# Optimization experiments

Hardware: AMD Instinct MI355X
Metric: run time of the kernel (lower is better)

Reference implementation:

```python
import jax, jax.numpy as jnp
import numpy as np
import math

D_MODEL = 1024
N_HEADS = 16
HEAD_DIM = D_MODEL // N_HEADS
B = 2
S = 2048

def setup_inputs() -> dict:
    key = jax.random.key(0)
    ks = jax.random.split(key, 5)
    x = jax.random.normal(ks[0], (B, S, D_MODEL), dtype=jnp.float32)
    # causal lower-triangular mask, broadcastable to [B, H, S, S]
    mask = jnp.tril(jnp.ones((S, S), dtype=bool))[None, None, :, :]
    # qkv_proj: Linear(d_model, 3*d_model); out_proj: Linear(d_model, d_model)
    lim_qkv = 1.0 / math.sqrt(D_MODEL)
    Wqkv = jax.random.uniform(ks[1], (D_MODEL, 3 * D_MODEL), minval=-lim_qkv, maxval=lim_qkv, dtype=jnp.float32)
    bqkv = jax.random.uniform(ks[2], (3 * D_MODEL,), minval=-lim_qkv, maxval=lim_qkv, dtype=jnp.float32)
    Wo = jax.random.uniform(ks[3], (D_MODEL, D_MODEL), minval=-lim_qkv, maxval=lim_qkv, dtype=jnp.float32)
    bo = jax.random.uniform(ks[4], (D_MODEL,), minval=-lim_qkv, maxval=lim_qkv, dtype=jnp.float32)
    return {"x": x, "mask": mask, "Wqkv": Wqkv, "bqkv": bqkv, "Wo": Wo, "bo": bo}

def reference(x, mask, Wqkv, bqkv, Wo, bo):
    b, s, d = x.shape
    scale = math.sqrt(HEAD_DIM)
    qkv = x @ Wqkv + bqkv                                   # [b, s, 3d]
    qkv = qkv.reshape(b, s, 3, N_HEADS, HEAD_DIM)
    qkv = jnp.transpose(qkv, (2, 0, 3, 1, 4))               # [3, b, h, s, hd]
    q, k, v = qkv[0], qkv[1], qkv[2]
    scores = jnp.einsum("bhqd,bhkd->bhqk", q, k) / scale    # [b, h, s, s]
    scores = jnp.where(mask, scores, -jnp.inf)
    attn = jax.nn.softmax(scores, axis=-1)                  # dropout inactive (eval)
    out = jnp.einsum("bhqk,bhkd->bhqd", attn, v)            # [b, h, s, hd]
    out = jnp.transpose(out, (0, 2, 1, 3)).reshape(b, s, d)
    return out @ Wo + bo
```

## Files before the change

kernel.cpp:

```cpp
#include <hip/hip_runtime.h>
#include <stdint.h>

typedef __bf16 bf16x8 __attribute__((ext_vector_type(8)));
typedef float  f32x4  __attribute__((ext_vector_type(4)));

__device__ __forceinline__ float bf2f(ushort u) {
    union { uint i; float f; } v; v.i = ((uint)u) << 16; return v.f;
}
__device__ __forceinline__ ushort f2bf(float f) {
    union { uint i; float f; } v; v.f = f;
    uint i = v.i;
    uint r = (i + 0x7fffu + ((i >> 16) & 1u)) >> 16;
    return (ushort)r;
}
__device__ __forceinline__ ushort f2bf_t(float f) {
    union { uint i; float f; } v; v.f = f;
    return (ushort)(v.i >> 16);
}

#if __has_builtin(__builtin_amdgcn_exp2f)
#define EXP2F __builtin_amdgcn_exp2f
#else
#define EXP2F exp2f
#endif

__device__ __forceinline__ void gld16(const ushort* g, ushort* l) {
    __builtin_amdgcn_global_load_lds((const __attribute__((address_space(1))) uint*)g,
                                     (__attribute__((address_space(3))) uint*)l, 16, 0, 0);
}

#define D_MODEL 1024
#define N_HEADS 16
#define HEAD_DIM 64
#define BATCH 2
#define SEQ 2048
#define M_ROWS (BATCH * SEQ)
#define N_ITEMS 1024
#define SCALE_LOG2E 0.18033688f

__global__ __launch_bounds__(256) void cast_f32_bf16(
    const float* __restrict__ in, ushort* __restrict__ out, int n4)
{
    int i = blockIdx.x * 256 + threadIdx.x;
    if (i < n4) {
        float4 v = ((const float4*)in)[i];
        ushort4 o;
        o.x = f2bf(v.x); o.y = f2bf(v.y); o.z = f2bf(v.z); o.w = f2bf(v.w);
        ((ushort4*)out)[i] = o;
    }
}

__global__ __launch_bounds__(256) void transpose_f32_bf16(
    const float* __restrict__ in, ushort* __restrict__ out, int K, int N)
{
    __shared__ float tile[64][65];
    const int k0 = blockIdx.y << 6, n0 = blockIdx.x << 6;
    const int tid = threadIdx.x;
    {
        const int r  = tid >> 4;
        const int c4 = (tid & 15) * 4;
#pragma unroll
        for (int rr = 0; rr < 4; ++rr) {
            int kk = r + rr * 16;
            float4 v = *(const float4*)(in + (size_t)(k0 + kk) * N + n0 + c4);
            tile[kk][c4 + 0] = v.x; tile[kk][c4 + 1] = v.y;
            tile[kk][c4 + 2] = v.z; tile[kk][c4 + 3] = v.w;
        }
    }
    __syncthreads();
    {
        const int nn = tid & 63;
        const int ch = tid >> 6;
#pragma unroll
        for (int cc = 0; cc < 2; ++cc) {
            int k8 = (ch + cc * 4) * 8;
            ushort tmp[8] __attribute__((aligned(16)));
#pragma unroll
            for (int j = 0; j < 8; ++j) tmp[j] = f2bf(tile[k8 + j][nn]);
            *(uint4*)(out + (size_t)(n0 + nn) * K + k0 + k8) = *(const uint4*)tmp;
        }
    }
}

__global__ __launch_bounds__(256) void gemm_bt128(
    const ushort* __restrict__ A, const ushort* __restrict__ Bt,
    const float* __restrict__ bias, float* __restrict__ out,
    ushort* __restrict__ Qb, ushort* __restrict__ Kb, ushort* __restrict__ Vb,
    int M, int N, int K, int mode)
{
    __shared__ ushort smem[64 * 136];
    ushort* As = smem;
    ushort* Bs = smem + 128 * 32;
    const int tid = threadIdx.x, lane = tid & 63, w = tid >> 6;
    const int wr = w >> 1, wc = w & 1;
    const int m0 = blockIdx.y * 128, n0 = blockIdx.x * 128;
    const int quad = lane >> 4, r15 = lane & 15, q8 = quad * 8;

    f32x4 acc[4][4] = {};

    const int cb0 = w * 64;
    const int cb1 = 256 + w * 64;
    const int c0 = cb0 + lane, c1 = cb1 + lane;
    const int row0 = c0 >> 2, sc0 = (c0 & 3) * 8;
    const int row1 = c1 >> 2, sc1 = (c1 & 3) * 8;

    for (int k0 = 0; k0 < K; k0 += 32) {
        gld16(A  + (size_t)(m0 + row0) * K + k0 + sc0, As + cb0 * 8);
        gld16(A  + (size_t)(m0 + row1) * K + k0 + sc1, As + cb1 * 8);
        gld16(Bt + (size_t)(n0 + row0) * K + k0 + sc0, Bs + cb0 * 8);
        gld16(Bt + (size_t)(n0 + row1) * K + k0 + sc1, Bs + cb1 * 8);
        __syncthreads();
        bf16x8 af[4], bfv[4];
#pragma unroll
        for (int mt = 0; mt < 4; ++mt)
            af[mt] = *(const bf16x8*)&As[(wr * 64 + mt * 16 + r15) * 32 + q8];
#pragma unroll
        for (int nt = 0; nt < 4; ++nt)
            bfv[nt] = *(const bf16x8*)&Bs[(wc * 64 + nt * 16 + r15) * 32 + q8];
#pragma unroll
        for (int mt = 0; mt < 4; ++mt)
#pragma unroll
            for (int nt = 0; nt < 4; ++nt)
                acc[mt][nt] = __builtin_amdgcn_mfma_f32_16x16x32_bf16(af[mt], bfv[nt], acc[mt][nt], 0, 0, 0);
        __syncthreads();
    }

    const int q4 = quad * 4;
    float bv[4];
#pragma unroll
    for (int nt = 0; nt < 4; ++nt) bv[nt] = bias[n0 + wc * 64 + nt * 16 + r15];

    if (mode == 0) {
        ushort* Cs = smem;
#pragma unroll
        for (int h = 0; h < 2; ++h) {
            __syncthreads();
            if (wr == h) {
#pragma unroll
                for (int mt = 0; mt < 4; ++mt)
#pragma unroll
                    for (int nt = 0; nt < 4; ++nt)
#pragma unroll
                        for (int r = 0; r < 4; ++r)
                            Cs[(mt * 16 + q4 + r) * 136 + wc * 64 + nt * 16 + r15] =
                                f2bf(acc[mt][nt][r] + bv[nt]);
            }
            __syncthreads();
#pragma unroll
            for (int it = 0; it < 4; ++it) {
                int idx = it * 256 + tid;
                int row = idx >> 4, chunk = idx & 15;
                int m = m0 + h * 64 + row;
                int n = n0 + chunk * 8;
                int which = n >> 10, nh = n & 1023;
                int hh = nh >> 6, d = nh & 63;
                int b = m >> 11, s = m & 2047;
                size_t dst = (((size_t)(b * N_HEADS + hh)) * SEQ + s) * HEAD_DIM + d;
                ushort* p = (which == 0) ? Qb : ((which == 1) ? Kb : Vb);
                *(uint4*)(p + dst) = *(const uint4*)&Cs[row * 136 + chunk * 8];
            }
        }
    } else {
        float* Cf = (float*)smem;
#pragma unroll
        for (int h = 0; h < 4; ++h) {
            __syncthreads();
            if (wr == (h >> 1)) {
                const int mtb = (h & 1) * 2;
#pragma unroll
                for (int mt2 = 0; mt2 < 2; ++mt2)
#pragma unroll
                    for (int nt = 0; nt < 4; ++nt)
#pragma unroll
                        for (int r = 0; r < 4; ++r)
                            Cf[(mt2 * 16 + q4 + r) * 136 + wc * 64 + nt * 16 + r15] =
                                acc[mtb + mt2][nt][r] + bv[nt];
            }
            __syncthreads();
#pragma unroll
            for (int it = 0; it < 4; ++it) {
                int idx = it * 256 + tid;
                int row = idx >> 5, chunk = idx & 31;
                float4 v = *(const float4*)&Cf[row * 136 + chunk * 4];
                int m = m0 + h * 32 + row;
                *(float4*)(out + (size_t)m * N + n0 + chunk * 4) = v;
            }
        }
    }
}

__global__ __launch_bounds__(256) void attn_mfma(
    const ushort* __restrict__ Q, const ushort* __restrict__ K,
    const ushort* __restrict__ V, ushort* __restrict__ Out,
    int* __restrict__ counter)
{
    __shared__ ushort Ks[2][64 * 72];
    __shared__ ushort Vt[2][64 * 72];
    __shared__ ushort Ps[4][16 * 72];
    __shared__ int s_item;

    const int tid  = threadIdx.x;
    const int lane = tid & 63;
    const int w    = tid >> 6;
    const int quad = lane >> 4;
    const int r15  = lane & 15;
    const int q8   = quad * 8;

    const int srow = tid >> 2;
    const int scol = (tid & 3) * 16;
    const int kp = tid & 31;
    const int dg = tid >> 5;

    for (;;) {
        __syncthreads();
        if (tid == 0) s_item = atomicAdd(counter, 1);
        __syncthreads();
        const int item = s_item;
        if (item >= N_ITEMS) break;

        const int qblk = 31 - (item >> 5);
        const int bh   = item & 31;
        const int q0   = qblk * 64;
        const size_t base = (size_t)bh * SEQ * HEAD_DIM;
        const int wq0  = q0 + w * 16;
        const int ntiles = qblk + 1;

        bf16x8 qf[2];
        {
            const ushort* qrow = Q + base + (size_t)(wq0 + r15) * HEAD_DIM;
            qf[0] = *(const bf16x8*)(qrow + q8);
            qf[1] = *(const bf16x8*)(qrow + 32 + q8);
        }

        f32x4 o_acc[4] = {};
        float l_lane[4] = {0.f, 0.f, 0.f, 0.f};

        uint4 kr0, kr1, vr0, vr1;
        {
            const ushort* kpt = K + base + (size_t)srow * HEAD_DIM + scol;
            kr0 = *(const uint4*)kpt; kr1 = *(const uint4*)(kpt + 8);
            const ushort* vpt = V + base + (size_t)(2 * kp) * HEAD_DIM + dg * 8;
            vr0 = *(const uint4*)vpt; vr1 = *(const uint4*)(vpt + HEAD_DIM);
        }
        {
            ushort* ks = &Ks[0][0];
            *(uint4*)&ks[srow * 72 + scol]     = kr0;
            *(uint4*)&ks[srow * 72 + scol + 8] = kr1;
            const ushort* a = (const ushort*)&vr0;
            const ushort* b = (const ushort*)&vr1;
            uint* vt32 = (uint*)&Vt[0][0];
#pragma unroll
            for (int j = 0; j < 8; ++j)
                vt32[(dg * 8 + j) * 36 + ((kp + 4 * dg) & 31)] = (uint)a[j] | ((uint)b[j] << 16);
        }
        if (ntiles > 1) {
            const ushort* kpt = K + base + (size_t)(64 + srow) * HEAD_DIM + scol;
            kr0 = *(const uint4*)kpt; kr1 = *(const uint4*)(kpt + 8);
            const ushort* vpt = V + base + (size_t)(64 + 2 * kp) * HEAD_DIM + dg * 8;
            vr0 = *(const uint4*)vpt; vr1 = *(const uint4*)(vpt + HEAD_DIM);
        }

        for (int t = 0; t < ntiles; ++t) {
            __syncthreads();
            if (t + 1 < ntiles) {
                const int b1 = (t + 1) & 1;
                ushort* ks = &Ks[b1][0];
                *(uint4*)&ks[srow * 72 + scol]     = kr0;
                *(uint4*)&ks[srow * 72 + scol + 8] = kr1;
                const ushort* a = (const ushort*)&vr0;
                const ushort* b = (const ushort*)&vr1;
                uint* vt32 = (uint*)&Vt[b1][0];
#pragma unroll
                for (int j = 0; j < 8; ++j)
                    vt32[(dg * 8 + j) * 36 + ((kp + 4 * dg) & 31)] = (uint)a[j] | ((uint)b[j] << 16);
            }
            if (t + 2 < ntiles) {
                const int key2 = (t + 2) << 6;
                const ushort* kpt = K + base + (size_t)(key2 + srow) * HEAD_DIM + scol;
                kr0 = *(const uint4*)kpt; kr1 = *(const uint4*)(kpt + 8);
                const ushort* vpt = V + base + (size_t)(key2 + 2 * kp) * HEAD_DIM + dg * 8;
                vr0 = *(const uint4*)vpt; vr1 = *(const uint4*)(vpt + HEAD_DIM);
            }

            const ushort* KsB = &Ks[t & 1][0];
            const ushort* VtB = &Vt[t & 1][0];
            const bool diag = (t == ntiles - 1);
            const int ntmax = diag ? (w + 1) : 4;

            f32x4 s_acc[4];
            __builtin_amdgcn_s_setprio(1);
#pragma unroll
            for (int nt = 0; nt < 4; ++nt) {
                if (nt >= ntmax) continue;
                f32x4 z = {};
#pragma unroll
                for (int ks = 0; ks < 2; ++ks) {
                    bf16x8 kf = *(const bf16x8*)&KsB[(nt * 16 + r15) * 72 + ks * 32 + q8];
                    z = __builtin_amdgcn_mfma_f32_16x16x32_bf16(qf[ks], kf, z, 0, 0, 0);
                }
                s_acc[nt] = z;
            }
            __builtin_amdgcn_s_setprio(0);
#pragma unroll
            for (int nt = 0; nt < 4; ++nt) {
                if (nt >= ntmax) continue;
#pragma unroll
                for (int j = 0; j < 4; ++j) {
                    float e = EXP2F(s_acc[nt][j] * SCALE_LOG2E);
                    if (diag && nt == w && r15 > quad * 4 + j) e = 0.f;
                    s_acc[nt][j] = e;
                    l_lane[j] += e;
                }
            }
            ushort* pb = &Ps[w][0];
#pragma unroll
            for (int nt = 0; nt < 4; ++nt)
#pragma unroll
                for (int j = 0; j < 4; ++j)
                    pb[(quad * 4 + j) * 72 + nt * 16 + r15] =
                        (nt < ntmax) ? f2bf_t(s_acc[nt][j]) : (ushort)0;
            bf16x8 pf0 = *(const bf16x8*)&pb[r15 * 72 + q8];
            bf16x8 pf1 = *(const bf16x8*)&pb[r15 * 72 + 32 + q8];

            __builtin_amdgcn_s_setprio(1);
#pragma unroll
            for (int nt = 0; nt < 4; ++nt) {
                const int d0 = nt * 16 + r15;
                const int dsw = 4 * ((d0 >> 3) & 7);
                const int c0 = (4 * quad + dsw) & 31;
                const int c1 = (16 + 4 * quad + dsw) & 31;
                bf16x8 vf0 = *(const bf16x8*)&VtB[d0 * 72 + (c0 << 1)];
                bf16x8 vf1 = *(const bf16x8*)&VtB[d0 * 72 + (c1 << 1)];
                o_acc[nt] = __builtin_amdgcn_mfma_f32_16x16x32_bf16(pf0, vf0, o_acc[nt], 0, 0, 0);
                o_acc[nt] = __builtin_amdgcn_mfma_f32_16x16x32_bf16(pf1, vf1, o_acc[nt], 0, 0, 0);
            }
            __builtin_amdgcn_s_setprio(0);
        }

        float l_f[4];
#pragma unroll
        for (int j = 0; j < 4; ++j) {
            float l = l_lane[j];
            l += __shfl_xor(l, 1);
            l += __shfl_xor(l, 2);
            l += __shfl_xor(l, 4);
            l += __shfl_xor(l, 8);
            l_f[j] = 1.f / l;
        }
        const int b = bh >> 4, h = bh & 15;
#pragma unroll
        for (int nt = 0; nt < 4; ++nt) {
#pragma unroll
            for (int j = 0; j < 4; ++j) {
                int qg = wq0 + quad * 4 + j;
                float v = o_acc[nt][j] * l_f[j];
                Out[((size_t)(b * SEQ + qg)) * D_MODEL + h * 64 + nt * 16 + r15] = f2bf(v);
            }
        }
    }
}

extern "C" void kernel_launch(void* const* d_in, const int* in_sizes, int n_in,
                              void* d_out, int out_size, void* d_ws, size_t ws_size,
                              hipStream_t stream)
{
    const float* x    = (const float*)d_in[0];
    const float* Wqkv = (const float*)d_in[2];
    const float* bqkv = (const float*)d_in[3];
    const float* Wo   = (const float*)d_in[4];
    const float* bo   = (const float*)d_in[5];
    float* out = (float*)d_out;

    char* ws = (char*)d_ws;
    size_t off = 0;
    ushort* xb    = (ushort*)(ws + off); off += (size_t)M_ROWS * D_MODEL * 2;
    ushort* WqkvT = (ushort*)(ws + off); off += (size_t)3 * D_MODEL * D_MODEL * 2;
    ushort* WoT   = (ushort*)(ws + off); off += (size_t)D_MODEL * D_MODEL * 2;
    const size_t qkv_elems = (size_t)BATCH * N_HEADS * SEQ * HEAD_DIM;
    ushort* Qb = (ushort*)(ws + off); off += qkv_elems * 2;
    ushort* Kb = (ushort*)(ws + off); off += qkv_elems * 2;
    ushort* Vb = (ushort*)(ws + off); off += qkv_elems * 2;
    ushort* attn_out = (ushort*)(ws + off); off += (size_t)M_ROWS * D_MODEL * 2;
    int* counter = (int*)(ws + off); off += 256;

    hipMemsetAsync(counter, 0, 4, stream);

    {
        int n4 = M_ROWS * D_MODEL / 4;
        cast_f32_bf16<<<(n4 + 255) / 256, 256, 0, stream>>>(x, xb, n4);
    }

    transpose_f32_bf16<<<dim3(3 * D_MODEL / 64, D_MODEL / 64), 256, 0, stream>>>(Wqkv, WqkvT, D_MODEL, 3 * D_MODEL);
    transpose_f32_bf16<<<dim3(D_MODEL / 64, D_MODEL / 64), 256, 0, stream>>>(Wo, WoT, D_MODEL, D_MODEL);

    gemm_bt128<<<dim3(3 * D_MODEL / 128, M_ROWS / 128), 256, 0, stream>>>(
        xb, WqkvT, bqkv, nullptr, Qb, Kb, Vb, M_ROWS, 3 * D_MODEL, D_MODEL, 0);

    attn_mfma<<<768, 256, 0, stream>>>(Qb, Kb, Vb, attn_out, counter);

    gemm_bt128<<<dim3(D_MODEL / 128, M_ROWS / 128), 256, 0, stream>>>(
        attn_out, WoT, bo, out, nullptr, nullptr, nullptr, M_ROWS, D_MODEL, D_MODEL, 1);
}
```

Measured before the change: 219.6 us.

## Keep attention probabilities in registers via transposed S and 16x16x16 MFMA

Computes S transposed (K as the A operand) so each lane's score fragment maps directly onto the A operand of a 16x16x16 bf16 MFMA for P·V. This removes the LDS round trip through the Ps buffer and its associated writes and reads, and reorganises the row-sum reduction to match the transposed layout. It also skips PV MFMAs for fully masked diagonal subtiles and raises the persistent grid from 768 to 1024 blocks. The tradeoff is twice as many smaller MFMA instructions for P·V, plus a fallback path kept for compilers lacking the builtin.

```diff
diff --git a/kernel.cpp b/kernel.cpp
--- a/kernel.cpp
+++ b/kernel.cpp
@@ -2,7 +2,17 @@
 #include <stdint.h>
 
 typedef __bf16 bf16x8 __attribute__((ext_vector_type(8)));
+typedef __bf16 bf16x4 __attribute__((ext_vector_type(4)));
+typedef short  s16x4  __attribute__((ext_vector_type(4)));
 typedef float  f32x4  __attribute__((ext_vector_type(4)));
+
+#if __has_builtin(__builtin_amdgcn_mfma_f32_16x16x16_bf16)
+#define HAVE_MFMA16 2
+#elif __has_builtin(__builtin_amdgcn_mfma_f32_16x16x16bf16_1k)
+#define HAVE_MFMA16 1
+#else
+#define HAVE_MFMA16 0
+#endif
 
 __device__ __forceinline__ float bf2f(ushort u) {
     union { uint i; float f; } v; v.i = ((uint)u) << 16; return v.f;
@@ -17,6 +27,20 @@
     union { uint i; float f; } v; v.f = f;
     return (ushort)(v.i >> 16);
 }
+__device__ __forceinline__ uint pack_bf2(float a, float b) {
+    union { uint i; float f; } va, vb; va.f = a; vb.f = b;
+    return (va.i >> 16) | (vb.i & 0xffff0000u);
+}
+
+#if HAVE_MFMA16
+__device__ __forceinline__ f32x4 mfma16(uint2 a, uint2 b, f32x4 c) {
+#if HAVE_MFMA16 == 2
+    return __builtin_amdgcn_mfma_f32_16x16x16_bf16(*(bf16x4*)&a, *(bf16x4*)&b, c, 0, 0, 0);
+#else
+    return __builtin_amdgcn_mfma_f32_16x16x16bf16_1k(*(s16x4*)&a, *(s16x4*)&b, c, 0, 0, 0);
+#endif
+}
+#endif
 
 #if __has_builtin(__builtin_amdgcn_exp2f)
 #define EXP2F __builtin_amdgcn_exp2f
@@ -196,7 +220,9 @@
 {
     __shared__ ushort Ks[2][64 * 72];
     __shared__ ushort Vt[2][64 * 72];
+#if !HAVE_MFMA16
     __shared__ ushort Ps[4][16 * 72];
+#endif
     __shared__ int s_item;
 
     const int tid  = threadIdx.x;
@@ -233,7 +259,11 @@
         }
 
         f32x4 o_acc[4] = {};
+#if HAVE_MFMA16
+        float l_sc = 0.f;
+#else
         float l_lane[4] = {0.f, 0.f, 0.f, 0.f};
+#endif
 
         uint4 kr0, kr1, vr0, vr1;
         {
@@ -287,6 +317,51 @@
             const bool diag = (t == ntiles - 1);
             const int ntmax = diag ? (w + 1) : 4;
 
+#if HAVE_MFMA16
+            f32x4 s_acc[4];
+            __builtin_amdgcn_s_setprio(1);
+#pragma unroll
+            for (int nt = 0; nt < 4; ++nt) {
+                if (nt >= ntmax) continue;
+                f32x4 z = {};
+#pragma unroll
+                for (int ks = 0; ks < 2; ++ks) {
+                    bf16x8 kf = *(const bf16x8*)&KsB[(nt * 16 + r15) * 72 + ks * 32 + q8];
+                    z = __builtin_amdgcn_mfma_f32_16x16x32_bf16(kf, qf[ks], z, 0, 0, 0);
+                }
+                s_acc[nt] = z;
+            }
+            __builtin_amdgcn_s_setprio(0);
+            uint2 pa[4];
+#pragma unroll
+            for (int nt = 0; nt < 4; ++nt) {
+                if (nt >= ntmax) continue;
+#pragma unroll
+                for (int j = 0; j < 4; ++j) {
+                    float e = EXP2F(s_acc[nt][j] * SCALE_LOG2E);
+                    if (diag && nt == w && quad * 4 + j > r15) e = 0.f;
+                    s_acc[nt][j] = e;
+                    l_sc += e;
+                }
+                pa[nt].x = pack_bf2(s_acc[nt][0], s_acc[nt][1]);
+                pa[nt].y = pack_bf2(s_acc[nt][2], s_acc[nt][3]);
+            }
+            __builtin_amdgcn_s_setprio(1);
+            const uint* vt32 = (const uint*)VtB;
+#pragma unroll
+            for (int ds = 0; ds < 4; ++ds) {
+                const int d = ds * 16 + r15;
+                const int rowb = d * 36 + ((4 * (d >> 3)) & 31);
+#pragma unroll
+                for (int nt = 0; nt < 4; ++nt) {
+                    if (nt >= ntmax) continue;
+                    const int cw = (nt * 8 + quad * 2 + 4 * (d >> 3)) & 31;
+                    uint2 vb = *(const uint2*)&vt32[d * 36 + cw];
+                    o_acc[ds] = mfma16(pa[nt], vb, o_acc[ds]);
+                }
+            }
+            __builtin_amdgcn_s_setprio(0);
+#else
             f32x4 s_acc[4];
             __builtin_amdgcn_s_setprio(1);
 #pragma unroll
@@ -335,9 +410,19 @@
                 o_acc[nt] = __builtin_amdgcn_mfma_f32_16x16x32_bf16(pf1, vf1, o_acc[nt], 0, 0, 0);
             }
             __builtin_amdgcn_s_setprio(0);
+#endif
         }
 
         float l_f[4];
+#if HAVE_MFMA16
+        float lt = l_sc + __shfl_xor(l_sc, 16);
+        lt += __shfl_xor(lt, 32);
+#pragma unroll
+        for (int j = 0; j < 4; ++j) {
+            float lq = __shfl(lt, (lane & 48) | (quad * 4 + j));
+            l_f[j] = 1.f / lq;
+        }
+#else
 #pragma unroll
         for (int j = 0; j < 4; ++j) {
             float l = l_lane[j];
@@ -347,6 +432,7 @@
             l += __shfl_xor(l, 8);
             l_f[j] = 1.f / l;
         }
+#endif
         const int b = bh >> 4, h = bh & 15;
 #pragma unroll
         for (int nt = 0; nt < 4; ++nt) {
@@ -396,7 +482,7 @@
     gemm_bt128<<<dim3(3 * D_MODEL / 128, M_ROWS / 128), 256, 0, stream>>>(
         xb, WqkvT, bqkv, nullptr, Qb, Kb, Vb, M_ROWS, 3 * D_MODEL, D_MODEL, 0);
 
-    attn_mfma<<<768, 256, 0, stream>>>(Qb, Kb, Vb, attn_out, counter);
+    attn_mfma<<<1024, 256, 0, stream>>>(Qb, Kb, Vb, attn_out, counter);
 
     gemm_bt128<<<dim3(D_MODEL / 128, M_ROWS / 128), 256, 0, stream>>>(
         attn_out, WoT, bo, out, nullptr, nullptr, nullptr, M_ROWS, D_MODEL, D_MODEL, 1);
```

After: 221.5 us. No clear change (+0.9%).
